# Optimization experiments

Hardware: AMD Instinct MI355X
Metric: run time of the kernel (lower is better)

Reference implementation:

```python
import jax, jax.numpy as jnp
import numpy as np

B, S, T = 16, 64, 64
H, V = 512, 32000


def _gru_step(h, x_t, W_ih, W_hh, b_ih, b_hh):
    # PyTorch GRU cell: gates ordered (r, z, n)
    gi = x_t @ W_ih.T + b_ih          # [B, 3H]
    gh = h @ W_hh.T + b_hh            # [B, 3H]
    i_r, i_z, i_n = jnp.split(gi, 3, axis=-1)
    h_r, h_z, h_n = jnp.split(gh, 3, axis=-1)
    r = jax.nn.sigmoid(i_r + h_r)
    z = jax.nn.sigmoid(i_z + h_z)
    n = jnp.tanh(i_n + r * h_n)
    return (1.0 - z) * n + z * h


def setup_inputs() -> dict:
    key = jax.random.key(0)
    ks = jax.random.split(key, 16)
    sc = 1.0 / np.sqrt(H)
    d = {
        'x': jax.random.randint(ks[0], (B, S), 0, V),
        'y': jax.random.randint(ks[1], (B, T), 0, V),
        'emb_enc': jax.random.normal(ks[2], (V, H), jnp.float32) * 0.02,
        'W_ih_e': jax.random.normal(ks[3], (3 * H, H), jnp.float32) * sc,
        'W_hh_e': jax.random.normal(ks[4], (3 * H, H), jnp.float32) * sc,
        'b_ih_e': jnp.zeros((3 * H,), jnp.float32),
        'b_hh_e': jnp.zeros((3 * H,), jnp.float32),
        'emb_dec': jax.random.normal(ks[5], (V, H), jnp.float32) * 0.02,
        'W_ih_d': jax.random.normal(ks[6], (3 * H, H), jnp.float32) * sc,
        'W_hh_d': jax.random.normal(ks[7], (3 * H, H), jnp.float32) * sc,
        'b_ih_d': jnp.zeros((3 * H,), jnp.float32),
        'b_hh_d': jnp.zeros((3 * H,), jnp.float32),
        'W_c': jax.random.normal(ks[8], (H, 2 * H), jnp.float32) * sc,
        'b_c': jnp.zeros((H,), jnp.float32),
        'W_out': jax.random.normal(ks[9], (V, H), jnp.float32) * sc,
        'b_out': jnp.zeros((V,), jnp.float32),
    }
    return d


def _forward(x, y, emb_enc, W_ih_e, W_hh_e, b_ih_e, b_hh_e,
             emb_dec, W_ih_d, W_hh_d, b_ih_d, b_hh_d,
             W_c, b_c, W_out, b_out):
    # ---- Encoder: GRU over source tokens (dropout=0 / eval) ----
    emb_x = emb_enc[x]                         # [B, S, H]
    def enc_step(h, e_t):
        h = _gru_step(h, e_t, W_ih_e, W_hh_e, b_ih_e, b_hh_e)
        return h, h
    h0 = jnp.zeros((x.shape[0], H), jnp.float32)
    h_enc, enc_seq = jax.lax.scan(enc_step, h0, jnp.swapaxes(emb_x, 0, 1))
    enc_out = jnp.swapaxes(enc_seq, 0, 1)      # [B, S, H]

    # ---- Decoder: teacher forcing (ratio=1.0), dot-product attention ----
    def dec_step(h, tok):
        e = emb_dec[tok]                                   # [B, H]
        h = _gru_step(h, e, W_ih_d, W_hh_d, b_ih_d, b_hh_d)
        score = jnp.einsum('bh,bsh->bs', h, enc_out)       # dot-product, unscaled
        w = jax.nn.softmax(score, axis=-1)
        attn = jnp.einsum('bs,bsh->bh', w, enc_out)        # [B, H]
        d = jnp.tanh(jnp.concatenate([h, attn], axis=-1) @ W_c.T + b_c)
        logits = d @ W_out.T + b_out                       # [B, V]
        return h, logits
    # decode steps use y[:, 0 .. T-2] as inputs, predict positions 1..T-1
    _, logits_seq = jax.lax.scan(dec_step, h_enc, jnp.swapaxes(y[:, :-1], 0, 1))
    logit = jnp.swapaxes(logits_seq, 0, 1)     # [B, T-1, V]

    tgt = y[:, 1:]
    logp = jax.nn.log_softmax(logit, axis=-1)
    nll = -jnp.take_along_axis(logp, tgt[..., None], axis=-1)[..., 0]
    loss = jnp.mean(nll)
    return logit, loss


def reference(x, y, emb_enc, W_ih_e, W_hh_e, b_ih_e, b_hh_e,
              emb_dec, W_ih_d, W_hh_d, b_ih_d, b_hh_d,
              W_c, b_c, W_out, b_out):
    return _forward(x, y, emb_enc, W_ih_e, W_hh_e, b_ih_e, b_hh_e,
                    emb_dec, W_ih_d, W_hh_d, b_ih_d, b_hh_d,
                    W_c, b_c, W_out, b_out)
```

## Files before the change

kernel.cpp:

```cpp
#include <hip/hip_runtime.h>

typedef unsigned short u16;
typedef unsigned int u32;
typedef __attribute__((ext_vector_type(8))) short short8;
typedef __attribute__((ext_vector_type(4))) float floatx4;

#define B_ 16
#define S_ 64
#define H_ 512
#define V_ 32000
#define G3 1536
#define TD 63
#define MROWS 1008
#define NBLK 16
#define NTILES 250

__device__ __forceinline__ float b2f(u16 u) {
  union { u32 i; float f; } c; c.i = ((u32)u) << 16; return c.f;
}
__device__ __forceinline__ u16 f2b(float f) {
  union { float f; u32 i; } c; c.f = f;
  u32 u = c.i;
  return (u16)((u + 0x7FFFu + ((u >> 16) & 1u)) >> 16);
}
__device__ __forceinline__ short8 pack8(float4 a, float4 b) {
  short8 r;
  r[0] = (short)f2b(a.x); r[1] = (short)f2b(a.y); r[2] = (short)f2b(a.z); r[3] = (short)f2b(a.w);
  r[4] = (short)f2b(b.x); r[5] = (short)f2b(b.y); r[6] = (short)f2b(b.z); r[7] = (short)f2b(b.w);
  return r;
}

template <int MODE, int SWAP = 0, int GATHER = 0>
__global__ void __launch_bounds__(256) gemm_bt(
    const u16* __restrict__ A, const float* __restrict__ Aemb,
    const int* __restrict__ idx, const float* __restrict__ Bm,
    const float* __restrict__ bias, void* __restrict__ Cout, int M, int N, int K,
    float* __restrict__ prtl, float* __restrict__ tokv, const int* __restrict__ yarr)
{
  __shared__ u16 As[64 * 40];
  __shared__ u16 Bs[128 * 40];
  const int tid = threadIdx.x;
  const int wave = tid >> 6, lane = tid & 63;
  const int l15 = lane & 15, quad = lane >> 4;
  const int m0 = (SWAP ? blockIdx.x : blockIdx.y) * 64;
  const int n0 = (SWAP ? blockIdx.y : blockIdx.x) * 128;
  floatx4 acc[4][2] = {};

  for (int kk = 0; kk < K; kk += 32) {
    {
      int row = tid >> 2, ch = tid & 3;
      short8 v = {};
      int gm = m0 + row;
      if (gm < M) {
        if (GATHER == 0) {
          v = *(const short8*)(A + (size_t)gm * K + kk + ch * 8);
        } else {
          int tok = (GATHER == 1) ? idx[gm] : idx[((gm & 15) << 6) + (gm >> 4)];
          const float* src = Aemb + (size_t)tok * 512 + kk + ch * 8;
          v = pack8(*(const float4*)src, *(const float4*)(src + 4));
        }
      }
      *(short8*)(As + row * 40 + ch * 8) = v;
    }
#pragma unroll
    for (int i = 0; i < 4; ++i) {
      int idx2 = tid + i * 256;
      int row = idx2 >> 3, c4 = idx2 & 7;
      int gn = n0 + row;
      float4 w = *(const float4*)(Bm + (size_t)gn * K + kk + c4 * 4);
      uint2 p;
      p.x = (u32)f2b(w.x) | ((u32)f2b(w.y) << 16);
      p.y = (u32)f2b(w.z) | ((u32)f2b(w.w) << 16);
      *(uint2*)(Bs + row * 40 + c4 * 4) = p;
    }
    __syncthreads();
    short8 af[4], bfr[2];
#pragma unroll
    for (int mt = 0; mt < 4; ++mt)
      af[mt] = *(const short8*)(As + (mt * 16 + l15) * 40 + quad * 8);
#pragma unroll
    for (int nt = 0; nt < 2; ++nt)
      bfr[nt] = *(const short8*)(Bs + (wave * 32 + nt * 16 + l15) * 40 + quad * 8);
#pragma unroll
    for (int mt = 0; mt < 4; ++mt)
#pragma unroll
      for (int nt = 0; nt < 2; ++nt)
        acc[mt][nt] = __builtin_amdgcn_mfma_f32_16x16x32_bf16(af[mt], bfr[nt], acc[mt][nt], 0, 0, 0);
    __syncthreads();
  }

  if (MODE == 1) {
    __shared__ float2 red[4][64];
    const int y0 = n0 >> 7;
#pragma unroll
    for (int mt = 0; mt < 4; ++mt) {
#pragma unroll
      for (int r = 0; r < 4; ++r) {
        const int gm = m0 + mt * 16 + quad * 4 + r;
        const int gn0 = n0 + wave * 32 + l15;
        float vv0 = acc[mt][0][r] + bias[gn0];
        float vv1 = acc[mt][1][r] + bias[gn0 + 16];
        if (gm < M) {
          const int tt = gm >> 4, bb = gm & 15;
          float* orow = (float*)Cout + ((size_t)bb * TD + tt) * V_;
          orow[gn0] = vv0;
          orow[gn0 + 16] = vv1;
          const int tok = yarr[bb * 64 + tt + 1];
          if (tok == gn0) tokv[gm] = vv0;
          if (tok == gn0 + 16) tokv[gm] = vv1;
        }
        float mx = fmaxf(vv0, vv1);
        float sm = __expf(vv0 - mx) + __expf(vv1 - mx);
#pragma unroll
        for (int d = 1; d < 16; d <<= 1) {
          const float om = __shfl_xor(mx, d), os = __shfl_xor(sm, d);
          const float nm = fmaxf(mx, om);
          sm = sm * __expf(mx - nm) + os * __expf(om - nm);
          mx = nm;
        }
        if (l15 == 0) red[wave][mt * 16 + quad * 4 + r] = make_float2(mx, sm);
      }
    }
    __syncthreads();
    if (tid < 64) {
      const float2 p0 = red[0][tid], p1 = red[1][tid], p2 = red[2][tid], p3 = red[3][tid];
      float M2 = fmaxf(fmaxf(p0.x, p1.x), fmaxf(p2.x, p3.x));
      float S2 = p0.y * __expf(p0.x - M2) + p1.y * __expf(p1.x - M2)
               + p2.y * __expf(p2.x - M2) + p3.y * __expf(p3.x - M2);
      const int gm = m0 + tid;
      if (gm < M) {
        float* pp = prtl + ((size_t)gm * NTILES + y0) * 2;
        pp[0] = M2; pp[1] = S2;
      }
    }
  } else {
#pragma unroll
    for (int mt = 0; mt < 4; ++mt) {
#pragma unroll
      for (int nt = 0; nt < 2; ++nt) {
        int gn = n0 + wave * 32 + nt * 16 + l15;
        float bv = bias[gn];
#pragma unroll
        for (int r = 0; r < 4; ++r) {
          int gm = m0 + mt * 16 + quad * 4 + r;
          if (gm < M) {
            float v = acc[mt][nt][r] + bv;
            if (MODE == 0) {
              ((float*)Cout)[(size_t)gm * N + gn] = v;
            } else {
              ((u16*)Cout)[(size_t)gm * N + gn] = f2b(tanhf(v));
            }
          }
        }
      }
    }
  }
}

struct RecArgs {
  const float* gi_enc;
  const float* gi_dec;
  const float* Whe;
  const float* Whd;
  const float* bhe;
  const float* bhd;
  u16* eo;
  u16* ha;
  u16* hcat;
  int* bar;
};

__device__ __forceinline__ void gridbar(int* slots, int gen) {
  __syncthreads();
  if (threadIdx.x < 16) {
    if (threadIdx.x == 0) {
      __builtin_amdgcn_fence(__ATOMIC_RELEASE, "agent");
      __hip_atomic_store(slots + (int)blockIdx.x * 32, gen, __ATOMIC_RELAXED, __HIP_MEMORY_SCOPE_AGENT);
    }
    while (__hip_atomic_load(slots + (int)threadIdx.x * 32, __ATOMIC_RELAXED, __HIP_MEMORY_SCOPE_AGENT) < gen) {}
    __builtin_amdgcn_fence(__ATOMIC_ACQUIRE, "agent");
  }
  __syncthreads();
}

template <int ISENC>
__device__ __forceinline__ void gate_phase(const RecArgs& a, int wave, int lane, int l15, int quad,
    int J, int step, int p, const short8* wf, float bh, float* hreg, const float* giv,
    float (&lds_rz)[2][2][16][16])
{
  const int sub = wave % 3, half = wave / 3;
  const int jc = J + half * 16 + l15;
  const u16* hb = a.ha + p * 8192 + l15 * 512 + quad * 8;
  short8 af[16];
#pragma unroll
  for (int kk = 0; kk < 16; ++kk) af[kk] = *(const short8*)(hb + kk * 32);
  floatx4 acc = {0.f, 0.f, 0.f, 0.f};
#pragma unroll
  for (int kk = 0; kk < 16; ++kk)
    acc = __builtin_amdgcn_mfma_f32_16x16x32_bf16(af[kk], wf[(ISENC ? 0 : 16) + kk], acc, 0, 0, 0);
  if (sub < 2) {
#pragma unroll
    for (int r = 0; r < 4; ++r)
      lds_rz[sub][half][quad * 4 + r][l15] = acc[r] + bh + giv[r];
    __syncthreads();
  } else {
    __syncthreads();
    const int pn = p ^ 1;
#pragma unroll
    for (int r = 0; r < 4; ++r) {
      const int b = quad * 4 + r;
      const float rp = lds_rz[0][half][b][l15];
      const float zp = lds_rz[1][half][b][l15];
      const float rr = 1.f / (1.f + __expf(-rp));
      const float zz = 1.f / (1.f + __expf(-zp));
      const float nn = tanhf(giv[r] + rr * (acc[r] + bh));
      const float hv = (1.f - zz) * nn + zz * hreg[r];
      hreg[r] = hv;
      const u16 h16 = f2b(hv);
      const u32 up = (u32)h16 | ((u32)(u16)__shfl_xor((int)h16, 1) << 16);
      if (!(lane & 1)) {
        *(u32*)(a.ha + pn * 8192 + b * 512 + jc) = up;
        if (ISENC) *(u32*)(a.eo + ((size_t)(b * 64 + step)) * 512 + jc) = up;
        else       *(u32*)(a.hcat + ((size_t)(step * 16 + b)) * 1024 + jc) = up;
      }
    }
  }
}

__global__ void __launch_bounds__(384) rec_kernel(RecArgs a) {
  __shared__ float lds_rz[2][2][16][16];
  const int tid = threadIdx.x;
  const int wave = tid >> 6, lane = tid & 63;
  const int l15 = lane & 15, quad = lane >> 4;
  const int J = blockIdx.x * 32;
  const int sub = wave % 3, half = wave / 3;

  short8 wf[32];
  const int row = sub * 512 + J + half * 16 + l15;
  const float* pe = a.Whe + (size_t)row * 512 + quad * 8;
  const float* pd = a.Whd + (size_t)row * 512 + quad * 8;
#pragma unroll
  for (int kk = 0; kk < 16; ++kk) {
    wf[kk]      = pack8(*(const float4*)(pe + kk * 32), *(const float4*)(pe + kk * 32 + 4));
    wf[16 + kk] = pack8(*(const float4*)(pd + kk * 32), *(const float4*)(pd + kk * 32 + 4));
  }
  const int jc = J + half * 16 + l15;
  const float bhe = a.bhe[sub * 512 + jc];
  const float bhd = a.bhd[sub * 512 + jc];

  float hreg[4] = {0.f, 0.f, 0.f, 0.f};
  float giv[4];
#pragma unroll
  for (int r = 0; r < 4; ++r)
    giv[r] = a.gi_enc[(size_t)((quad * 4 + r) * 64) * G3 + sub * 512 + jc];

  if (sub == 2 && !(lane & 1)) {
#pragma unroll
    for (int r = 0; r < 4; ++r)
      *(u32*)(a.ha + (quad * 4 + r) * 512 + jc) = 0u;
  }
  int gen = 0;
  gridbar(a.bar, ++gen);

  for (int s = 0; s < S_; ++s) {
    gate_phase<1>(a, wave, lane, l15, quad, J, s, s & 1, wf, bhe, hreg, giv, lds_rz);
    if (s < S_ - 1) {
#pragma unroll
      for (int r = 0; r < 4; ++r)
        giv[r] = a.gi_enc[((size_t)((quad * 4 + r) * 64 + s + 1)) * G3 + sub * 512 + jc];
    } else {
#pragma unroll
      for (int r = 0; r < 4; ++r)
        giv[r] = a.gi_dec[((size_t)(quad * 4 + r)) * G3 + sub * 512 + jc];
    }
    gridbar(a.bar, ++gen);
  }

  for (int t = 0; t < TD; ++t) {
    gate_phase<0>(a, wave, lane, l15, quad, J, t, t & 1, wf, bhd, hreg, giv, lds_rz);
    if (t < TD - 1) {
#pragma unroll
      for (int r = 0; r < 4; ++r)
        giv[r] = a.gi_dec[((size_t)((t + 1) * 16 + quad * 4 + r)) * G3 + sub * 512 + jc];
      gridbar(a.bar, ++gen);
    }
  }
}

__global__ void __launch_bounds__(512) attn_kernel(
    const u16* __restrict__ eo16, u16* __restrict__ hcat)
{
  __shared__ float sc[64][9];
  __shared__ float wts[64];
  const int m = blockIdx.x, b = m & 15;
  const int tid = threadIdx.x;
  const u16* eo = eo16 + (size_t)b * 64 * 512;
  const u16* h = hcat + (size_t)m * 1024;
  {
    const int s = tid >> 3, q = tid & 7;
    const u16* ep = eo + s * 512 + q * 64;
    const u16* hp = h + q * 64;
    float acc = 0.f;
#pragma unroll
    for (int u = 0; u < 8; ++u) {
      short8 e8 = *(const short8*)(ep + u * 8);
      short8 h8 = *(const short8*)(hp + u * 8);
#pragma unroll
      for (int i = 0; i < 8; ++i) acc += b2f((u16)e8[i]) * b2f((u16)h8[i]);
    }
    sc[s][q] = acc;
  }
  __syncthreads();
  if (tid < 64) {
    float v = 0.f;
#pragma unroll
    for (int u = 0; u < 8; ++u) v += sc[tid][u];
    float mx = v;
#pragma unroll
    for (int d = 1; d < 64; d <<= 1) mx = fmaxf(mx, __shfl_xor(mx, d));
    float e = __expf(v - mx);
    float sum = e;
#pragma unroll
    for (int d = 1; d < 64; d <<= 1) sum += __shfl_xor(sum, d);
    wts[tid] = e / sum;
  }
  __syncthreads();
  {
    const int j = tid;
    float acc = 0.f;
#pragma unroll 8
    for (int s2 = 0; s2 < 64; ++s2) acc += wts[s2] * b2f(eo[s2 * 512 + j]);
    hcat[(size_t)m * 1024 + 512 + j] = f2b(acc);
  }
}

__global__ void __launch_bounds__(64) loss_merge_kernel(
    const float* __restrict__ prtl, const float* __restrict__ tokv, float* __restrict__ nll)
{
  const int m = blockIdx.x;
  const int lane = threadIdx.x;
  float mx = -1e30f, sm = 0.f;
  for (int i = lane; i < NTILES; i += 64) {
    const float pm = prtl[((size_t)m * NTILES + i) * 2];
    const float ps = prtl[((size_t)m * NTILES + i) * 2 + 1];
    const float nm = fmaxf(mx, pm);
    sm = sm * __expf(mx - nm) + ps * __expf(pm - nm);
    mx = nm;
  }
#pragma unroll
  for (int d = 1; d < 64; d <<= 1) {
    const float om = __shfl_xor(mx, d), os = __shfl_xor(sm, d);
    const float nm = fmaxf(mx, om);
    sm = sm * __expf(mx - nm) + os * __expf(om - nm);
    mx = nm;
  }
  if (lane == 0) nll[m] = mx + logf(sm) - tokv[m];
}

__global__ void __launch_bounds__(256) loss_final_kernel(const float* __restrict__ nll, float* __restrict__ out) {
  __shared__ float wred[4];
  const int tid = threadIdx.x;
  float s = 0.f;
  for (int i = tid; i < MROWS; i += 256) s += nll[i];
#pragma unroll
  for (int d = 1; d < 64; d <<= 1) s += __shfl_xor(s, d);
  if ((tid & 63) == 0) wred[tid >> 6] = s;
  __syncthreads();
  if (tid == 0) out[0] = (wred[0] + wred[1] + wred[2] + wred[3]) / 1008.f;
}

extern "C" void kernel_launch(void* const* d_in, const int* in_sizes, int n_in,
                              void* d_out, int out_size, void* d_ws, size_t ws_size,
                              hipStream_t stream)
{
  const int*   x       = (const int*)d_in[0];
  const int*   y       = (const int*)d_in[1];
  const float* emb_enc = (const float*)d_in[2];
  const float* W_ih_e  = (const float*)d_in[3];
  const float* W_hh_e  = (const float*)d_in[4];
  const float* b_ih_e  = (const float*)d_in[5];
  const float* b_hh_e  = (const float*)d_in[6];
  const float* emb_dec = (const float*)d_in[7];
  const float* W_ih_d  = (const float*)d_in[8];
  const float* W_hh_d  = (const float*)d_in[9];
  const float* b_ih_d  = (const float*)d_in[10];
  const float* b_hh_d  = (const float*)d_in[11];
  const float* W_c     = (const float*)d_in[12];
  const float* b_c     = (const float*)d_in[13];
  const float* W_out   = (const float*)d_in[14];
  const float* b_out   = (const float*)d_in[15];

  char* ws = (char*)d_ws;
  float* gi_enc = (float*)(ws + 0);
  float* gi_dec = (float*)(ws + 6291456);
  u16* hcat     = (u16*)(ws + 12484608);
  u16* Dm       = (u16*)(ws + 14565376);
  u16* eo16     = (u16*)(ws + 15597568);
  u16* ha16     = (u16*)(ws + 16646144);
  float* nll    = (float*)(ws + 16678912);
  int* bar      = (int*)(ws + 16682944);
  float* prtl   = (float*)(ws + 0);
  float* tokv   = (float*)(ws + 2016000);

  hipMemsetAsync(bar, 0, 2048, stream);

  gemm_bt<0, 0, 1><<<dim3(12, 16), dim3(256), 0, stream>>>(
      nullptr, emb_enc, x, W_ih_e, b_ih_e, (void*)gi_enc, 1024, G3, 512, nullptr, nullptr, nullptr);
  gemm_bt<0, 0, 2><<<dim3(12, 16), dim3(256), 0, stream>>>(
      nullptr, emb_dec, y, W_ih_d, b_ih_d, (void*)gi_dec, MROWS, G3, 512, nullptr, nullptr, nullptr);

  RecArgs ra{gi_enc, gi_dec, W_hh_e, W_hh_d, b_hh_e, b_hh_d, eo16, ha16, hcat, bar};
  rec_kernel<<<dim3(NBLK), dim3(384), 0, stream>>>(ra);

  attn_kernel<<<dim3(MROWS), dim3(512), 0, stream>>>(eo16, hcat);

  gemm_bt<2><<<dim3(4, 16), dim3(256), 0, stream>>>(
      hcat, nullptr, nullptr, W_c, b_c, (void*)Dm, MROWS, 512, 1024, nullptr, nullptr, nullptr);

  gemm_bt<1, 1><<<dim3(16, NTILES), dim3(256), 0, stream>>>(
      Dm, nullptr, nullptr, W_out, b_out, d_out, MROWS, V_, 512, prtl, tokv, y);

  loss_merge_kernel<<<dim3(MROWS), dim3(64), 0, stream>>>(prtl, tokv, nll);
  loss_final_kernel<<<dim3(1), dim3(256), 0, stream>>>(nll, ((float*)d_out) + (size_t)MROWS * V_);
}
```

Baseline: 1.339 ms.

## Replace grid barrier with per-wave flag polling and pre-gather embeddings

The recurrent kernel's full grid barrier (two syncthreads plus a fence) is replaced by per-half-block flags. The gate-producing waves write them after their hidden-state stores drain, and every wave polls all 32 flags before reading h through coherent atomic loads. This removes block-wide syncs and fences from the serial critical path of 127 steps, at the cost of weaker memory-ordering guarantees. Separately, embedding lookups are pulled out of the input-projection GEMMs into a gather kernel that writes bf16 rows, which adds an extra launch.

```diff
diff --git a/kernel.cpp b/kernel.cpp
--- a/kernel.cpp
+++ b/kernel.cpp
@@ -2,6 +2,7 @@
 
 typedef unsigned short u16;
 typedef unsigned int u32;
+typedef unsigned long long u64;
 typedef __attribute__((ext_vector_type(8))) short short8;
 typedef __attribute__((ext_vector_type(4))) float floatx4;
 
@@ -30,10 +31,34 @@
   return r;
 }
 
-template <int MODE, int SWAP = 0, int GATHER = 0>
+__device__ __forceinline__ short8 ld_bf8_coh(const u16* p) {
+  u64 a = __hip_atomic_load((const u64*)p, __ATOMIC_RELAXED, __HIP_MEMORY_SCOPE_AGENT);
+  u64 b = __hip_atomic_load((const u64*)(p + 4), __ATOMIC_RELAXED, __HIP_MEMORY_SCOPE_AGENT);
+  union { u64 q[2]; short8 s; } u; u.q[0] = a; u.q[1] = b; return u.s;
+}
+
+__global__ void __launch_bounds__(256) gather_kernel(
+    const int* __restrict__ x, const int* __restrict__ y,
+    const float* __restrict__ emb_enc, const float* __restrict__ emb_dec,
+    u16* __restrict__ ex, u16* __restrict__ ey)
+{
+  const int r = blockIdx.x, tid = threadIdx.x;
+  if (r < B_ * S_) {
+    int tok = x[r];
+    float2 v = ((const float2*)(emb_enc + (size_t)tok * H_))[tid];
+    ((u32*)(ex + (size_t)r * H_))[tid] = (u32)f2b(v.x) | ((u32)f2b(v.y) << 16);
+  } else {
+    int m = r - B_ * S_;
+    int t = m >> 4, b = m & 15;
+    int tok = y[b * 64 + t];
+    float2 v = ((const float2*)(emb_dec + (size_t)tok * H_))[tid];
+    ((u32*)(ey + (size_t)m * H_))[tid] = (u32)f2b(v.x) | ((u32)f2b(v.y) << 16);
+  }
+}
+
+template <int MODE, int SWAP = 0>
 __global__ void __launch_bounds__(256) gemm_bt(
-    const u16* __restrict__ A, const float* __restrict__ Aemb,
-    const int* __restrict__ idx, const float* __restrict__ Bm,
+    const u16* __restrict__ A, const float* __restrict__ Bm,
     const float* __restrict__ bias, void* __restrict__ Cout, int M, int N, int K,
     float* __restrict__ prtl, float* __restrict__ tokv, const int* __restrict__ yarr)
 {
@@ -51,15 +76,7 @@
       int row = tid >> 2, ch = tid & 3;
       short8 v = {};
       int gm = m0 + row;
-      if (gm < M) {
-        if (GATHER == 0) {
-          v = *(const short8*)(A + (size_t)gm * K + kk + ch * 8);
-        } else {
-          int tok = (GATHER == 1) ? idx[gm] : idx[((gm & 15) << 6) + (gm >> 4)];
-          const float* src = Aemb + (size_t)tok * 512 + kk + ch * 8;
-          v = pack8(*(const float4*)src, *(const float4*)(src + 4));
-        }
-      }
+      if (gm < M) v = *(const short8*)(A + (size_t)gm * K + kk + ch * 8);
       *(short8*)(As + row * 40 + ch * 8) = v;
     }
 #pragma unroll
@@ -170,30 +187,30 @@
   int* bar;
 };
 
-__device__ __forceinline__ void gridbar(int* slots, int gen) {
-  __syncthreads();
-  if (threadIdx.x < 16) {
-    if (threadIdx.x == 0) {
-      __builtin_amdgcn_fence(__ATOMIC_RELEASE, "agent");
-      __hip_atomic_store(slots + (int)blockIdx.x * 32, gen, __ATOMIC_RELAXED, __HIP_MEMORY_SCOPE_AGENT);
-    }
-    while (__hip_atomic_load(slots + (int)threadIdx.x * 32, __ATOMIC_RELAXED, __HIP_MEMORY_SCOPE_AGENT) < gen) {}
-    __builtin_amdgcn_fence(__ATOMIC_ACQUIRE, "agent");
-  }
-  __syncthreads();
+__device__ __forceinline__ void pollbar(int* slots, int lane, int gen) {
+  while (__hip_atomic_load(slots + (lane & 31) * 32, __ATOMIC_RELAXED, __HIP_MEMORY_SCOPE_AGENT) < gen) {}
+  asm volatile("" ::: "memory");
 }
 
 template <int ISENC>
 __device__ __forceinline__ void gate_phase(const RecArgs& a, int wave, int lane, int l15, int quad,
-    int J, int step, int p, const short8* wf, float bh, float* hreg, const float* giv,
-    float (&lds_rz)[2][2][16][16])
+    int J, int step, int p, const short8* wf, float bh, float* hreg,
+    float (&lds_rz)[2][2][16][16], int signal_gen, bool do_signal)
 {
   const int sub = wave % 3, half = wave / 3;
   const int jc = J + half * 16 + l15;
+  const float* gi = ISENC ? a.gi_enc : a.gi_dec;
+  float giv[4];
+#pragma unroll
+  for (int r = 0; r < 4; ++r) {
+    const int b = quad * 4 + r;
+    const int row = ISENC ? (b * 64 + step) : (step * 16 + b);
+    giv[r] = gi[(size_t)row * G3 + sub * 512 + jc];
+  }
   const u16* hb = a.ha + p * 8192 + l15 * 512 + quad * 8;
   short8 af[16];
 #pragma unroll
-  for (int kk = 0; kk < 16; ++kk) af[kk] = *(const short8*)(hb + kk * 32);
+  for (int kk = 0; kk < 16; ++kk) af[kk] = ld_bf8_coh(hb + kk * 32);
   floatx4 acc = {0.f, 0.f, 0.f, 0.f};
 #pragma unroll
   for (int kk = 0; kk < 16; ++kk)
@@ -219,10 +236,17 @@
       const u16 h16 = f2b(hv);
       const u32 up = (u32)h16 | ((u32)(u16)__shfl_xor((int)h16, 1) << 16);
       if (!(lane & 1)) {
-        *(u32*)(a.ha + pn * 8192 + b * 512 + jc) = up;
+        __hip_atomic_store((u32*)(a.ha + pn * 8192 + b * 512 + jc), up,
+                           __ATOMIC_RELAXED, __HIP_MEMORY_SCOPE_AGENT);
         if (ISENC) *(u32*)(a.eo + ((size_t)(b * 64 + step)) * 512 + jc) = up;
         else       *(u32*)(a.hcat + ((size_t)(step * 16 + b)) * 1024 + jc) = up;
       }
+    }
+    if (do_signal) {
+      asm volatile("s_waitcnt vmcnt(0)" ::: "memory");
+      if (lane == 0)
+        __hip_atomic_store(a.bar + ((int)blockIdx.x * 2 + half) * 32, signal_gen,
+                           __ATOMIC_RELAXED, __HIP_MEMORY_SCOPE_AGENT);
     }
   }
 }
@@ -249,41 +273,30 @@
   const float bhd = a.bhd[sub * 512 + jc];
 
   float hreg[4] = {0.f, 0.f, 0.f, 0.f};
-  float giv[4];
-#pragma unroll
-  for (int r = 0; r < 4; ++r)
-    giv[r] = a.gi_enc[(size_t)((quad * 4 + r) * 64) * G3 + sub * 512 + jc];
-
-  if (sub == 2 && !(lane & 1)) {
-#pragma unroll
-    for (int r = 0; r < 4; ++r)
-      *(u32*)(a.ha + (quad * 4 + r) * 512 + jc) = 0u;
-  }
-  int gen = 0;
-  gridbar(a.bar, ++gen);
-
+
+  if (sub == 2) {
+    if (!(lane & 1)) {
+#pragma unroll
+      for (int r = 0; r < 4; ++r)
+        __hip_atomic_store((u32*)(a.ha + (quad * 4 + r) * 512 + jc), 0u,
+                           __ATOMIC_RELAXED, __HIP_MEMORY_SCOPE_AGENT);
+    }
+    asm volatile("s_waitcnt vmcnt(0)" ::: "memory");
+    if (lane == 0)
+      __hip_atomic_store(a.bar + ((int)blockIdx.x * 2 + half) * 32, 1,
+                         __ATOMIC_RELAXED, __HIP_MEMORY_SCOPE_AGENT);
+  }
+
+  int gen = 1;
   for (int s = 0; s < S_; ++s) {
-    gate_phase<1>(a, wave, lane, l15, quad, J, s, s & 1, wf, bhe, hreg, giv, lds_rz);
-    if (s < S_ - 1) {
-#pragma unroll
-      for (int r = 0; r < 4; ++r)
-        giv[r] = a.gi_enc[((size_t)((quad * 4 + r) * 64 + s + 1)) * G3 + sub * 512 + jc];
-    } else {
-#pragma unroll
-      for (int r = 0; r < 4; ++r)
-        giv[r] = a.gi_dec[((size_t)(quad * 4 + r)) * G3 + sub * 512 + jc];
-    }
-    gridbar(a.bar, ++gen);
-  }
-
+    pollbar(a.bar, lane, gen);
+    gate_phase<1>(a, wave, lane, l15, quad, J, s, s & 1, wf, bhe, hreg, lds_rz, gen + 1, true);
+    ++gen;
+  }
   for (int t = 0; t < TD; ++t) {
-    gate_phase<0>(a, wave, lane, l15, quad, J, t, t & 1, wf, bhd, hreg, giv, lds_rz);
-    if (t < TD - 1) {
-#pragma unroll
-      for (int r = 0; r < 4; ++r)
-        giv[r] = a.gi_dec[((size_t)((t + 1) * 16 + quad * 4 + r)) * G3 + sub * 512 + jc];
-      gridbar(a.bar, ++gen);
-    }
+    pollbar(a.bar, lane, gen);
+    gate_phase<0>(a, wave, lane, l15, quad, J, t, t & 1, wf, bhd, hreg, lds_rz, gen + 1, t < TD - 1);
+    ++gen;
   }
 }
 
@@ -393,6 +406,8 @@
   char* ws = (char*)d_ws;
   float* gi_enc = (float*)(ws + 0);
   float* gi_dec = (float*)(ws + 6291456);
+  u16* embx     = (u16*)(ws + 12484608);
+  u16* emby     = (u16*)(ws + 13533184);
   u16* hcat     = (u16*)(ws + 12484608);
   u16* Dm       = (u16*)(ws + 14565376);
   u16* eo16     = (u16*)(ws + 15597568);
@@ -402,12 +417,14 @@
   float* prtl   = (float*)(ws + 0);
   float* tokv   = (float*)(ws + 2016000);
 
-  hipMemsetAsync(bar, 0, 2048, stream);
-
-  gemm_bt<0, 0, 1><<<dim3(12, 16), dim3(256), 0, stream>>>(
-      nullptr, emb_enc, x, W_ih_e, b_ih_e, (void*)gi_enc, 1024, G3, 512, nullptr, nullptr, nullptr);
-  gemm_bt<0, 0, 2><<<dim3(12, 16), dim3(256), 0, stream>>>(
-      nullptr, emb_dec, y, W_ih_d, b_ih_d, (void*)gi_dec, MROWS, G3, 512, nullptr, nullptr, nullptr);
+  hipMemsetAsync(bar, 0, 4096, stream);
+
+  gather_kernel<<<dim3(B_ * S_ + MROWS), dim3(256), 0, stream>>>(x, y, emb_enc, emb_dec, embx, emby);
+
+  gemm_bt<0><<<dim3(12, 16), dim3(256), 0, stream>>>(
+      embx, W_ih_e, b_ih_e, (void*)gi_enc, 1024, G3, 512, nullptr, nullptr, nullptr);
+  gemm_bt<0><<<dim3(12, 16), dim3(256), 0, stream>>>(
+      emby, W_ih_d, b_ih_d, (void*)gi_dec, MROWS, G3, 512, nullptr, nullptr, nullptr);
 
   RecArgs ra{gi_enc, gi_dec, W_hh_e, W_hh_d, b_hh_e, b_hh_d, eo16, ha16, hcat, bar};
   rec_kernel<<<dim3(NBLK), dim3(384), 0, stream>>>(ra);
@@ -415,10 +432,10 @@
   attn_kernel<<<dim3(MROWS), dim3(512), 0, stream>>>(eo16, hcat);
 
   gemm_bt<2><<<dim3(4, 16), dim3(256), 0, stream>>>(
-      hcat, nullptr, nullptr, W_c, b_c, (void*)Dm, MROWS, 512, 1024, nullptr, nullptr, nullptr);
+      hcat, W_c, b_c, (void*)Dm, MROWS, 512, 1024, nullptr, nullptr, nullptr);
 
   gemm_bt<1, 1><<<dim3(16, NTILES), dim3(256), 0, stream>>>(
-      Dm, nullptr, nullptr, W_out, b_out, d_out, MROWS, V_, 512, prtl, tokv, y);
+      Dm, W_out, b_out, d_out, MROWS, V_, 512, prtl, tokv, y);
 
   loss_merge_kernel<<<dim3(MROWS), dim3(64), 0, stream>>>(prtl, tokv, nll);
   loss_final_kernel<<<dim3(1), dim3(256), 0, stream>>>(nll, ((float*)d_out) + (size_t)MROWS * V_);
```

Measured after the change: 1.593 ms. 1.19x slower.
